# Performance work log

Measured on AMD Instinct MI355X. Metric: run time of the kernel, lower is better.

The kernel has to match this reference:

```python
import jax, jax.numpy as jnp
import numpy as np

L, H, NH, NKV, HD, FF, V = 2, 2048, 16, 2, 128, 11008, 32000
B, S, R, LORA_SCALE = 32, 64, 16, 2.0  # lora scaling = alpha/r = 32/16
PH, TD = 1024, 512
ROPE_THETA = 1e6

def _rms(x, w, eps=1e-6):
    return x * jax.lax.rsqrt(jnp.mean(x * x, axis=-1, keepdims=True) + eps) * w

def _rot_half(x):
    h = x.shape[-1] // 2
    return jnp.concatenate([-x[..., h:], x[..., :h]], axis=-1)

def _lora_linear(x, W, A, Bm, b=None):
    y = x @ W.T + LORA_SCALE * ((x @ A.T) @ Bm.T)
    return y + b if b is not None else y

def _forward(input_ids, attention_mask, embed, Wq, bq, Aq, Bq, Wk, bk, Ak, Bk,
             Wv, bv, Av, Bv, Wo, Ao, Bo, ln1, ln2, Wg, Wu, Wd, norm_f,
             W1, b1, W2, b2):
    Bsz, Sl = input_ids.shape
    h = embed[input_ids]                                            # [B,S,H]
    inv_freq = 1.0 / (ROPE_THETA ** (jnp.arange(0, HD, 2, dtype=jnp.float32) / HD))
    ang = jnp.arange(Sl, dtype=jnp.float32)[:, None] * inv_freq      # [S,HD/2]
    cos = jnp.concatenate([jnp.cos(ang)] * 2, -1)[None, :, None, :]  # [1,S,1,HD]
    sin = jnp.concatenate([jnp.sin(ang)] * 2, -1)[None, :, None, :]
    causal = jnp.tril(jnp.ones((Sl, Sl), dtype=bool))
    keep = causal[None, None] & (attention_mask[:, None, None, :] > 0)
    bias = jnp.where(keep, 0.0, -1e9).astype(jnp.float32)            # [B,1,S,S]
    for l in range(L):
        x = _rms(h, ln1[l])
        q = _lora_linear(x, Wq[l], Aq[l], Bq[l], bq[l]).reshape(Bsz, Sl, NH, HD)
        k = _lora_linear(x, Wk[l], Ak[l], Bk[l], bk[l]).reshape(Bsz, Sl, NKV, HD)
        v = _lora_linear(x, Wv[l], Av[l], Bv[l], bv[l]).reshape(Bsz, Sl, NKV, HD)
        q = q * cos + _rot_half(q) * sin
        k = k * cos + _rot_half(k) * sin
        k = jnp.repeat(k, NH // NKV, axis=2)                         # GQA expand
        v = jnp.repeat(v, NH // NKV, axis=2)
        scores = jnp.einsum('bqhd,bkhd->bhqk', q, k) / np.sqrt(HD).astype(np.float32) + bias
        p = jax.nn.softmax(scores, axis=-1)
        attn = jnp.einsum('bhqk,bkhd->bqhd', p, v).reshape(Bsz, Sl, H)
        h = h + _lora_linear(attn, Wo[l], Ao[l], Bo[l])
        x = _rms(h, ln2[l])
        h = h + (jax.nn.silu(x @ Wg[l].T) * (x @ Wu[l].T)) @ Wd[l].T  # SwiGLU MLP
    h = _rms(h, norm_f)                       # final norm -> hidden_states[-1]
    seq_len = jnp.sum(attention_mask, axis=1) - 1
    pooled = h[jnp.arange(Bsz), seq_len]      # last valid token  [B,H]
    z = jax.nn.gelu(pooled @ W1.T + b1, approximate=False)
    return (z @ W2.T + b2).astype(jnp.float32)  # [B,512]

def setup_inputs():
    key = jax.random.key(0)
    ks = jax.random.split(key, 32)
    def n(k, shape, s=0.02):
        return (s * jax.random.normal(k, shape)).astype(jnp.float32)
    lens = jax.random.randint(ks[0], (B,), 1, S + 1)
    return {
        'input_ids': jax.random.randint(ks[1], (B, S), 0, V, dtype=jnp.int32),
        'attention_mask': (jnp.arange(S)[None, :] < lens[:, None]).astype(jnp.int32),
        'embed': n(ks[2], (V, H)),
        'Wq': n(ks[3], (L, H, H)), 'bq': n(ks[4], (L, H)),
        'Aq': n(ks[5], (L, R, H)), 'Bq': n(ks[6], (L, H, R)),
        'Wk': n(ks[7], (L, NKV * HD, H)), 'bk': n(ks[8], (L, NKV * HD)),
        'Ak': n(ks[9], (L, R, H)), 'Bk': n(ks[10], (L, NKV * HD, R)),
        'Wv': n(ks[11], (L, NKV * HD, H)), 'bv': n(ks[12], (L, NKV * HD)),
        'Av': n(ks[13], (L, R, H)), 'Bv': n(ks[14], (L, NKV * HD, R)),
        'Wo': n(ks[15], (L, H, H)),
        'Ao': n(ks[16], (L, R, H)), 'Bo': n(ks[17], (L, H, R)),
        'ln1': jnp.ones((L, H), jnp.float32), 'ln2': jnp.ones((L, H), jnp.float32),
        'Wg': n(ks[18], (L, FF, H)), 'Wu': n(ks[19], (L, FF, H)), 'Wd': n(ks[20], (L, H, FF)),
        'norm_f': jnp.ones((H,), jnp.float32),
        'W1': n(ks[21], (PH, H)), 'b1': jnp.zeros((PH,), jnp.float32),
        'W2': n(ks[22], (TD, PH)), 'b2': jnp.zeros((TD,), jnp.float32),
    }

def reference(input_ids, attention_mask, embed, Wq, bq, Aq, Bq, Wk, bk, Ak, Bk,
              Wv, bv, Av, Bv, Wo, Ao, Bo, ln1, ln2, Wg, Wu, Wd, norm_f,
              W1, b1, W2, b2):
    return _forward(input_ids, attention_mask, embed, Wq, bq, Aq, Bq, Wk, bk, Ak, Bk,
                    Wv, bv, Av, Bv, Wo, Ao, Bo, ln1, ln2, Wg, Wu, Wd, norm_f,
                    W1, b1, W2, b2)
```

## Files before the change

### kernel.cpp

```cpp
#include <hip/hip_runtime.h>
#include <hip/hip_bf16.h>
#include <math.h>

namespace {
constexpr int NL  = 2;
constexpr int H   = 2048;
constexpr int NH  = 16;
constexpr int NKV = 2;
constexpr int HD  = 128;
constexpr int FF  = 11008;
constexpr int BB  = 32;
constexpr int SS  = 64;
constexpr int RR  = 16;
constexpr int TT  = BB * SS;
constexpr int KVD = NKV * HD;
constexpr int QKVD = H + 2 * KVD;
constexpr int PH  = 1024, TDm = 512;
constexpr float LSCALE = 2.0f;
}

typedef __bf16 bf16x8 __attribute__((ext_vector_type(8)));
typedef float  f32x4  __attribute__((ext_vector_type(4)));

__device__ __forceinline__ ushort4 f4_to_bf4(float4 r) {
  __hip_bfloat16 a = __float2bfloat16(r.x), b = __float2bfloat16(r.y),
                 c = __float2bfloat16(r.z), d = __float2bfloat16(r.w);
  return make_ushort4(*(unsigned short*)&a, *(unsigned short*)&b,
                      *(unsigned short*)&c, *(unsigned short*)&d);
}

__device__ __forceinline__ bf16x8 f8cvt(float4 a, float4 b) {
  bf16x8 r;
  r[0] = (__bf16)a.x; r[1] = (__bf16)a.y; r[2] = (__bf16)a.z; r[3] = (__bf16)a.w;
  r[4] = (__bf16)b.x; r[5] = (__bf16)b.y; r[6] = (__bf16)b.z; r[7] = (__bf16)b.w;
  return r;
}

__device__ __forceinline__ float dot4(float4 a, float4 b) {
  return a.x * b.x + a.y * b.y + a.z * b.z + a.w * b.w;
}

__global__ __launch_bounds__(256) void k_embed(const int* __restrict__ ids,
                                               const float* __restrict__ emb,
                                               float* __restrict__ h) {
  int t = blockIdx.x;
  long id = ids[t];
  const float4* src = reinterpret_cast<const float4*>(emb + id * (long)H);
  float4* dst = reinterpret_cast<float4*>(h + (long)t * H);
  for (int i = threadIdx.x; i < H / 4; i += 256) dst[i] = src[i];
}

__global__ __launch_bounds__(256) void k_cvt(const float* __restrict__ src,
                                             __hip_bfloat16* __restrict__ dst, long n) {
  long i = ((long)blockIdx.x * 256 + threadIdx.x) * 4;
  if (i >= n) return;
  float4 v = *reinterpret_cast<const float4*>(src + i);
  *reinterpret_cast<ushort4*>(dst + i) = f4_to_bf4(v);
}

__global__ __launch_bounds__(256) void k_prep(
    const float* __restrict__ bq, const float* __restrict__ bk, const float* __restrict__ bv,
    const float* __restrict__ Bq, const float* __restrict__ Bk, const float* __restrict__ Bv,
    float* __restrict__ biascat, float* __restrict__ bcat) {
  int idx = blockIdx.x * 256 + threadIdx.x;
  if (idx >= NL * QKVD) return;
  int l = idx / QKVD, col = idx % QKVD;
  const float* bsrc; const float* Bsrc;
  if (col < H)            { bsrc = bq + (long)l * H + col;            Bsrc = Bq + ((long)l * H + col) * RR; }
  else if (col < H + KVD) { bsrc = bk + (long)l * KVD + (col - H);    Bsrc = Bk + ((long)l * KVD + col - H) * RR; }
  else                    { bsrc = bv + (long)l * KVD + (col - H - KVD); Bsrc = Bv + ((long)l * KVD + col - H - KVD) * RR; }
  biascat[idx] = *bsrc;
  #pragma unroll
  for (int r = 0; r < RR; ++r) bcat[(long)idx * RR + r] = Bsrc[r];
}

__global__ __launch_bounds__(256) void k_rmsnorm(const float* __restrict__ in,
                                                 const float* __restrict__ w,
                                                 float* __restrict__ out,
                                                 __hip_bfloat16* __restrict__ outb) {
  int t = blockIdx.x, tid = threadIdx.x;
  const float4* xr = reinterpret_cast<const float4*>(in + (long)t * H);
  float4 v0 = xr[tid], v1 = xr[tid + 256];
  float ss = v0.x*v0.x + v0.y*v0.y + v0.z*v0.z + v0.w*v0.w
           + v1.x*v1.x + v1.y*v1.y + v1.z*v1.z + v1.w*v1.w;
  #pragma unroll
  for (int off = 32; off; off >>= 1) ss += __shfl_xor(ss, off);
  __shared__ float sred[4];
  if ((tid & 63) == 0) sred[tid >> 6] = ss;
  __syncthreads();
  float scale = rsqrtf((sred[0] + sred[1] + sred[2] + sred[3]) * (1.0f / H) + 1e-6f);
  const float4* wr = reinterpret_cast<const float4*>(w);
  float4 w0 = wr[tid], w1 = wr[tid + 256];
  float4 r0 = make_float4(v0.x*scale*w0.x, v0.y*scale*w0.y, v0.z*scale*w0.z, v0.w*scale*w0.w);
  float4 r1 = make_float4(v1.x*scale*w1.x, v1.y*scale*w1.y, v1.z*scale*w1.z, v1.w*scale*w1.w);
  float4* o = reinterpret_cast<float4*>(out + (long)t * H);
  o[tid] = r0; o[tid + 256] = r1;
  ushort4* ob = reinterpret_cast<ushort4*>(outb + (long)t * H);
  ob[tid] = f4_to_bf4(r0); ob[tid + 256] = f4_to_bf4(r1);
}

enum { ME_BIAS_F32 = 0, ME_ACC_F32 = 1 };

__device__ __forceinline__ int raster_sw(int bid, int nwg) {
  int q8 = nwg >> 3, r8 = nwg & 7;
  int xcd = bid & 7, pos = bid >> 3;
  return (xcd < r8 ? xcd * (q8 + 1) : r8 * (q8 + 1) + (xcd - r8) * q8) + pos;
}

template <int EPI, bool LORA, bool WBF16>
__global__ __launch_bounds__(256, 3) void k_mgemm(
    const __hip_bfloat16* __restrict__ Abf,
    const float* __restrict__ W0, const float* __restrict__ W1, const float* __restrict__ W2,
    const __hip_bfloat16* __restrict__ Wb,
    const float* __restrict__ bias,
    float* __restrict__ Cf,
    const float* __restrict__ lt, const float* __restrict__ lB, int ltStride,
    int qkvMode, int M, int N, int K) {
  constexpr int BM = 64, BN = 128, BK = 64;
  constexpr int FM = 4, FN = 2;
  __shared__ __align__(16) __bf16 As[2][BM * BK];
  __shared__ __align__(16) __bf16 Bs[2][BN * BK];
  const int tid = threadIdx.x;
  const int sw = raster_sw(blockIdx.x, gridDim.x);
  const int ntm = M / BM;
  const int bm = (sw % ntm) * BM, bn = (sw / ntm) * BN;
  const int lane = tid & 63, wv = tid >> 6;
  const int wn = wv * 32;
  const int lr15 = lane & 15;
  const int g4 = lane >> 4;
  f32x4 acc[FM][FN] = {};
  const __bf16* Ag = reinterpret_cast<const __bf16*>(Abf) + (long)bm * K;

  const float* Wsrc = W0; int wrow0 = bn;
  if constexpr (!WBF16) {
    if (qkvMode) {
      if (bn >= H + KVD)      { Wsrc = W2; wrow0 = bn - (H + KVD); }
      else if (bn >= H)       { Wsrc = W1; wrow0 = bn - H; }
    }
  }
  const __bf16* Wg16 = reinterpret_cast<const __bf16*>(Wb) + (long)bn * K;

  const int arow = tid >> 3, acol = tid & 7;

  auto stageA = [&](int buf, int k0) {
    __builtin_amdgcn_global_load_lds(
        (const __attribute__((address_space(1))) void*)
          (Ag + (long)arow * K + k0 + ((acol ^ (arow & 7)) << 3)),
        (__attribute__((address_space(3))) void*)(&As[buf][tid * 8]), 16, 0, 0);
    int r1 = arow + 32;
    __builtin_amdgcn_global_load_lds(
        (const __attribute__((address_space(1))) void*)
          (Ag + (long)r1 * K + k0 + ((acol ^ (r1 & 7)) << 3)),
        (__attribute__((address_space(3))) void*)(&As[buf][(tid + 256) * 8]), 16, 0, 0);
  };

  auto stageB16 = [&](int buf, int k0) {
    #pragma unroll
    for (int q = 0; q < 4; ++q) {
      int c = tid + q * 256;
      int row = c >> 3, col = c & 7;
      __builtin_amdgcn_global_load_lds(
          (const __attribute__((address_space(1))) void*)
            (Wg16 + (long)row * K + k0 + ((col ^ (row & 7)) << 3)),
          (__attribute__((address_space(3))) void*)(&Bs[buf][c * 8]), 16, 0, 0);
    }
  };

  float4 bb[4][2];
  auto loadB = [&](int k0) {
    #pragma unroll
    for (int q = 0; q < 4; ++q) {
      int r = arow + q * 32;
      const float* p = Wsrc + (long)(wrow0 + r) * K + k0 + ((acol ^ (r & 7)) << 3);
      bb[q][0] = *reinterpret_cast<const float4*>(p);
      bb[q][1] = *reinterpret_cast<const float4*>(p + 4);
    }
  };
  auto writeB = [&](int buf) {
    #pragma unroll
    for (int q = 0; q < 4; ++q)
      *reinterpret_cast<bf16x8*>(&Bs[buf][(tid + q * 256) * 8]) = f8cvt(bb[q][0], bb[q][1]);
  };

  auto compute = [&](int buf) {
    #pragma unroll
    for (int ks = 0; ks < 2; ++ks) {
      bf16x8 af[FM], bfr[FN];
      #pragma unroll
      for (int m = 0; m < FM; ++m) {
        int row = m * 16 + lr15;
        af[m] = *reinterpret_cast<const bf16x8*>(
            &As[buf][row * BK + (((g4 + 4 * ks) ^ (row & 7)) << 3)]);
      }
      #pragma unroll
      for (int n = 0; n < FN; ++n) {
        int row = wn + n * 16 + lr15;
        bfr[n] = *reinterpret_cast<const bf16x8*>(
            &Bs[buf][row * BK + (((g4 + 4 * ks) ^ (row & 7)) << 3)]);
      }
      #pragma unroll
      for (int m = 0; m < FM; ++m)
        #pragma unroll
        for (int n = 0; n < FN; ++n)
          acc[m][n] = __builtin_amdgcn_mfma_f32_16x16x32_bf16(af[m], bfr[n], acc[m][n], 0, 0, 0);
    }
  };

  const int NS = K / BK;
  if constexpr (WBF16) {
    stageA(0, 0); stageB16(0, 0);
    __syncthreads();
    int cur = 0;
    for (int t = 0; t < NS; ++t) {
      if (t + 1 < NS) { stageA(cur ^ 1, (t + 1) * BK); stageB16(cur ^ 1, (t + 1) * BK); }
      compute(cur);
      if (t + 1 < NS) { __syncthreads(); cur ^= 1; }
    }
  } else {
    loadB(0);
    stageA(0, 0);
    writeB(0);
    __syncthreads();
    int cur = 0;
    for (int t = 0; t < NS; ++t) {
      if (t + 1 < NS) { loadB((t + 1) * BK); stageA(cur ^ 1, (t + 1) * BK); }
      compute(cur);
      if (t + 1 < NS) {
        writeB(cur ^ 1);
        __syncthreads();
        cur ^= 1;
      }
    }
  }

  const int r0 = g4 << 2;
  float4 lb[FN][4];
  int goff = 0;
  if constexpr (LORA) {
    if (qkvMode) goff = (bn >= H + KVD) ? 32 : (bn >= H ? 16 : 0);
    #pragma unroll
    for (int n = 0; n < FN; ++n) {
      const float4* p = reinterpret_cast<const float4*>(lB + (long)(bn + wn + n * 16 + lr15) * RR);
      lb[n][0] = p[0]; lb[n][1] = p[1]; lb[n][2] = p[2]; lb[n][3] = p[3];
    }
  }
  float bcol[FN];
  if constexpr (EPI == ME_BIAS_F32) {
    #pragma unroll
    for (int n = 0; n < FN; ++n) bcol[n] = bias[bn + wn + n * 16 + lr15];
  }
  #pragma unroll
  for (int m = 0; m < FM; ++m)
    #pragma unroll
    for (int j = 0; j < 4; ++j) {
      const long row = bm + m * 16 + r0 + j;
      float lv[FN];
      if constexpr (LORA) {
        const float4* tp = reinterpret_cast<const float4*>(lt + row * ltStride + goff);
        float4 t0 = tp[0], t1 = tp[1], t2 = tp[2], t3 = tp[3];
        #pragma unroll
        for (int n = 0; n < FN; ++n)
          lv[n] = LSCALE * (dot4(t0, lb[n][0]) + dot4(t1, lb[n][1]) +
                            dot4(t2, lb[n][2]) + dot4(t3, lb[n][3]));
      }
      #pragma unroll
      for (int n = 0; n < FN; ++n) {
        const int col = bn + wn + n * 16 + lr15;
        float v = acc[m][n][j];
        if constexpr (LORA) v += lv[n];
        if constexpr (EPI == ME_BIAS_F32) Cf[row * N + col] = v + bcol[n];
        else                              Cf[row * N + col] += v;
      }
    }
}

__global__ __launch_bounds__(256, 2) void k_swiglu_b(
    const __hip_bfloat16* __restrict__ Abf,
    const __hip_bfloat16* __restrict__ Wgb,
    const __hip_bfloat16* __restrict__ Wub,
    __hip_bfloat16* __restrict__ Cb,
    int M, int N, int K) {
  constexpr int BM = 128, BN = 128, BK = 32;
  constexpr int FM = 4, FN = 4;
  constexpr int ACH = BM * BK / 8;
  __shared__ __align__(16) __bf16 As[2][BM * BK];
  __shared__ __align__(16) __bf16 Gs[2][BN * BK];
  __shared__ __align__(16) __bf16 Us[2][BN * BK];
  const int tid = threadIdx.x;
  const int sw = raster_sw(blockIdx.x, gridDim.x);
  const int ntm = M / BM;
  const int bm = (sw % ntm) * BM, bn = (sw / ntm) * BN;
  const int lane = tid & 63, wv = tid >> 6;
  const int wm = (wv >> 1) * 64, wn = (wv & 1) * 64;
  const int lr15 = lane & 15;
  const int lks = (((lane >> 4) << 3)) ^ ((((lr15 >> 1) & 3)) << 3);
  f32x4 accg[FM][FN] = {}, accu[FM][FN] = {};
  const __bf16* Ag = reinterpret_cast<const __bf16*>(Abf) + (long)bm * K;
  const __bf16* Gg = reinterpret_cast<const __bf16*>(Wgb) + (long)bn * K;
  const __bf16* Ug = reinterpret_cast<const __bf16*>(Wub) + (long)bn * K;

  auto stage = [&](int buf, int k0) {
    #pragma unroll
    for (int i = tid; i < ACH; i += 256) {
      const int sc = ((i & 3) ^ ((i >> 3) & 3)) << 3;
      const long ro = (long)(i >> 2) * K + k0 + sc;
      __builtin_amdgcn_global_load_lds(
          (const __attribute__((address_space(1))) void*)(Ag + ro),
          (__attribute__((address_space(3))) void*)(&As[buf][i * 8]), 16, 0, 0);
      __builtin_amdgcn_global_load_lds(
          (const __attribute__((address_space(1))) void*)(Gg + ro),
          (__attribute__((address_space(3))) void*)(&Gs[buf][i * 8]), 16, 0, 0);
      __builtin_amdgcn_global_load_lds(
          (const __attribute__((address_space(1))) void*)(Ug + ro),
          (__attribute__((address_space(3))) void*)(&Us[buf][i * 8]), 16, 0, 0);
    }
  };
  auto compute = [&](int buf) {
    bf16x8 af[FM], gf[FN], uf[FN];
    #pragma unroll
    for (int m = 0; m < FM; ++m)
      af[m] = *reinterpret_cast<const bf16x8*>(&As[buf][(wm + m * 16 + lr15) * BK + lks]);
    #pragma unroll
    for (int n = 0; n < FN; ++n) {
      gf[n] = *reinterpret_cast<const bf16x8*>(&Gs[buf][(wn + n * 16 + lr15) * BK + lks]);
      uf[n] = *reinterpret_cast<const bf16x8*>(&Us[buf][(wn + n * 16 + lr15) * BK + lks]);
    }
    #pragma unroll
    for (int m = 0; m < FM; ++m)
      #pragma unroll
      for (int n = 0; n < FN; ++n) {
        accg[m][n] = __builtin_amdgcn_mfma_f32_16x16x32_bf16(af[m], gf[n], accg[m][n], 0, 0, 0);
        accu[m][n] = __builtin_amdgcn_mfma_f32_16x16x32_bf16(af[m], uf[n], accu[m][n], 0, 0, 0);
      }
  };

  const int NS = K / BK;
  stage(0, 0);
  asm volatile("s_waitcnt vmcnt(0)" ::: "memory");
  __builtin_amdgcn_s_barrier();
  int cur = 0;
  for (int t = 0; t < NS; ++t) {
    if (t + 1 < NS) stage(cur ^ 1, (t + 1) * BK);
    compute(cur);
    if (t + 1 < NS) {
      asm volatile("s_waitcnt vmcnt(0)" ::: "memory");
      __builtin_amdgcn_s_barrier();
      cur ^= 1;
    }
  }

  const int r0 = (lane >> 4) << 2;
  #pragma unroll
  for (int m = 0; m < FM; ++m)
    #pragma unroll
    for (int n = 0; n < FN; ++n) {
      const int col = bn + wn + n * 16 + lr15;
      const long rowb = bm + wm + m * 16 + r0;
      #pragma unroll
      for (int j = 0; j < 4; ++j) {
        float g = accg[m][n][j], u = accu[m][n][j];
        Cb[(rowb + j) * N + col] = __float2bfloat16((g / (1.0f + expf(-g))) * u);
      }
    }
}

__global__ __launch_bounds__(256, 2) void k_swiglu(
    const __hip_bfloat16* __restrict__ Abf,
    const float* __restrict__ Wg,
    const float* __restrict__ Wu,
    __hip_bfloat16* __restrict__ Cb,
    int M, int N, int K) {
  constexpr int BM = 128, BN = 128, BK = 32;
  constexpr int FM = 4, FN = 4;
  __shared__ __align__(16) __bf16 As[2][BM * BK];
  __shared__ __align__(16) __bf16 Gs[2][BN * BK];
  __shared__ __align__(16) __bf16 Us[2][BN * BK];
  const int tid = threadIdx.x;
  const int sw = raster_sw(blockIdx.x, gridDim.x);
  const int ntm = M / BM;
  const int bm = (sw % ntm) * BM, bn = (sw / ntm) * BN;
  const int lane = tid & 63, wv = tid >> 6;
  const int wm = (wv >> 1) * 64, wn = (wv & 1) * 64;
  const int lr15 = lane & 15;
  const int lks = (((lane >> 4) << 3)) ^ ((((lr15 >> 1) & 3)) << 3);
  f32x4 accg[FM][FN] = {}, accu[FM][FN] = {};
  const __bf16* Ag = reinterpret_cast<const __bf16*>(Abf) + (long)bm * K;

  const int br0 = tid >> 2, bc = tid & 3;
  const int br1 = br0 + 64;
  const float* gp0 = Wg + (long)(bn + br0) * K + bc * 8;
  const float* gp1 = Wg + (long)(bn + br1) * K + bc * 8;
  const float* up0 = Wu + (long)(bn + br0) * K + bc * 8;
  const float* up1 = Wu + (long)(bn + br1) * K + bc * 8;
  const int d0 = br0 * BK + ((bc ^ ((br0 >> 1) & 3)) << 3);
  const int d1 = br1 * BK + ((bc ^ ((br1 >> 1) & 3)) << 3);

  float4 g00, g01, g10, g11, u00, u01, u10, u11;
  auto loadB = [&](int k0) {
    g00 = *reinterpret_cast<const float4*>(gp0 + k0);
    g01 = *reinterpret_cast<const float4*>(gp0 + k0 + 4);
    g10 = *reinterpret_cast<const float4*>(gp1 + k0);
    g11 = *reinterpret_cast<const float4*>(gp1 + k0 + 4);
    u00 = *reinterpret_cast<const float4*>(up0 + k0);
    u01 = *reinterpret_cast<const float4*>(up0 + k0 + 4);
    u10 = *reinterpret_cast<const float4*>(up1 + k0);
    u11 = *reinterpret_cast<const float4*>(up1 + k0 + 4);
  };
  auto writeB = [&](int buf) {
    *reinterpret_cast<bf16x8*>(&Gs[buf][d0]) = f8cvt(g00, g01);
    *reinterpret_cast<bf16x8*>(&Gs[buf][d1]) = f8cvt(g10, g11);
    *reinterpret_cast<bf16x8*>(&Us[buf][d0]) = f8cvt(u00, u01);
    *reinterpret_cast<bf16x8*>(&Us[buf][d1]) = f8cvt(u10, u11);
  };
  auto stageA = [&](int buf, int k0) {
    #pragma unroll
    for (int i = tid; i < BM * BK / 8; i += 256)
      __builtin_amdgcn_global_load_lds(
          (const __attribute__((address_space(1))) void*)
            (Ag + (long)(i >> 2) * K + k0 + (((i & 3) ^ ((i >> 3) & 3)) << 3)),
          (__attribute__((address_space(3))) void*)(&As[buf][i * 8]), 16, 0, 0);
  };
  auto compute = [&](int buf) {
    bf16x8 af[FM], gf[FN], uf[FN];
    #pragma unroll
    for (int m = 0; m < FM; ++m)
      af[m] = *reinterpret_cast<const bf16x8*>(&As[buf][(wm + m * 16 + lr15) * BK + lks]);
    #pragma unroll
    for (int n = 0; n < FN; ++n) {
      gf[n] = *reinterpret_cast<const bf16x8*>(&Gs[buf][(wn + n * 16 + lr15) * BK + lks]);
      uf[n] = *reinterpret_cast<const bf16x8*>(&Us[buf][(wn + n * 16 + lr15) * BK + lks]);
    }
    #pragma unroll
    for (int m = 0; m < FM; ++m)
      #pragma unroll
      for (int n = 0; n < FN; ++n) {
        accg[m][n] = __builtin_amdgcn_mfma_f32_16x16x32_bf16(af[m], gf[n], accg[m][n], 0, 0, 0);
        accu[m][n] = __builtin_amdgcn_mfma_f32_16x16x32_bf16(af[m], uf[n], accu[m][n], 0, 0, 0);
      }
  };

  const int NS = K / BK;
  loadB(0);
  stageA(0, 0);
  writeB(0);
  __syncthreads();
  int cur = 0;
  for (int t = 0; t < NS; ++t) {
    if (t + 1 < NS) { loadB((t + 1) * BK); stageA(cur ^ 1, (t + 1) * BK); }
    compute(cur);
    if (t + 1 < NS) {
      writeB(cur ^ 1);
      __syncthreads();
      cur ^= 1;
    }
  }

  const int r0 = (lane >> 4) << 2;
  #pragma unroll
  for (int m = 0; m < FM; ++m)
    #pragma unroll
    for (int n = 0; n < FN; ++n) {
      const int col = bn + wn + n * 16 + lr15;
      const long rowb = bm + wm + m * 16 + r0;
      #pragma unroll
      for (int j = 0; j < 4; ++j) {
        float g = accg[m][n][j], u = accu[m][n][j];
        Cb[(rowb + j) * N + col] = __float2bfloat16((g / (1.0f + expf(-g))) * u);
      }
    }
}

enum { EPI_STORE = 0, EPI_GELU = 3 };

template <int EPI, bool HAS_BIAS>
__global__ __launch_bounds__(256) void k_gemm(const float* __restrict__ A,
                                              const float* __restrict__ W,
                                              const float* __restrict__ bias,
                                              float* __restrict__ C,
                                              int M, int N, int K) {
  constexpr int BM = 64, BN = 64, BK = 16;
  __shared__ float As[BK][BM + 4];
  __shared__ float Ws[BK][BN + 4];
  const int bm = blockIdx.y * BM, bn = blockIdx.x * BN;
  const int tid = threadIdx.x;
  const int lr = tid >> 2;
  const int lc = (tid & 3) << 2;
  const int ty = tid >> 4, tx = tid & 15;
  float acc[4][4] = {};
  const int arow = bm + lr;
  const bool aok = arow < M;
  const float* Ap = A + (long)arow * K + lc;
  const float* Wp = W + (long)(bn + lr) * K + lc;
  for (int k0 = 0; k0 < K; k0 += BK) {
    float4 av = aok ? *reinterpret_cast<const float4*>(Ap + k0) : make_float4(0.f, 0.f, 0.f, 0.f);
    float4 wv = *reinterpret_cast<const float4*>(Wp + k0);
    As[lc + 0][lr] = av.x; As[lc + 1][lr] = av.y; As[lc + 2][lr] = av.z; As[lc + 3][lr] = av.w;
    Ws[lc + 0][lr] = wv.x; Ws[lc + 1][lr] = wv.y; Ws[lc + 2][lr] = wv.z; Ws[lc + 3][lr] = wv.w;
    __syncthreads();
    #pragma unroll
    for (int k = 0; k < BK; ++k) {
      float4 a4 = *reinterpret_cast<const float4*>(&As[k][ty << 2]);
      float4 b4 = *reinterpret_cast<const float4*>(&Ws[k][tx << 2]);
      float a[4] = {a4.x, a4.y, a4.z, a4.w};
      float b[4] = {b4.x, b4.y, b4.z, b4.w};
      #pragma unroll
      for (int i = 0; i < 4; ++i)
        #pragma unroll
        for (int j = 0; j < 4; ++j) acc[i][j] = fmaf(a[i], b[j], acc[i][j]);
    }
    __syncthreads();
  }
  const int col = bn + (tx << 2);
  #pragma unroll
  for (int i = 0; i < 4; ++i) {
    int row = bm + (ty << 2) + i;
    if (row < M) {
      float4 r = make_float4(acc[i][0], acc[i][1], acc[i][2], acc[i][3]);
      if (HAS_BIAS) {
        float4 bv = *reinterpret_cast<const float4*>(bias + col);
        r.x += bv.x; r.y += bv.y; r.z += bv.z; r.w += bv.w;
      }
      if (EPI == EPI_GELU) {
        r.x = 0.5f * r.x * (1.0f + erff(r.x * 0.70710678118654752f));
        r.y = 0.5f * r.y * (1.0f + erff(r.y * 0.70710678118654752f));
        r.z = 0.5f * r.z * (1.0f + erff(r.z * 0.70710678118654752f));
        r.w = 0.5f * r.w * (1.0f + erff(r.w * 0.70710678118654752f));
      }
      *reinterpret_cast<float4*>(C + (long)row * N + col) = r;
    }
  }
}

__global__ __launch_bounds__(256) void k_lora_down3(
    const float* __restrict__ x,
    const float* __restrict__ A0, const float* __restrict__ A1, const float* __restrict__ A2,
    float* __restrict__ out, int outStride) {
  int t = blockIdx.x, g = blockIdx.y, tid = threadIdx.x;
  const float* A = (g == 0) ? A0 : (g == 1) ? A1 : A2;
  int r = tid & 15, sl = tid >> 4;
  const float* xr = x + (long)t * H + sl * 128;
  const float* Ar = A + (long)r * H + sl * 128;
  float p = 0.f;
  #pragma unroll 8
  for (int kk = 0; kk < 128; kk += 4) {
    float4 xv = *reinterpret_cast<const float4*>(xr + kk);
    float4 av = *reinterpret_cast<const float4*>(Ar + kk);
    p = fmaf(xv.x, av.x, p); p = fmaf(xv.y, av.y, p);
    p = fmaf(xv.z, av.z, p); p = fmaf(xv.w, av.w, p);
  }
  __shared__ float red[16][17];
  red[sl][r] = p;
  __syncthreads();
  if (tid < 16) {
    float s = 0.f;
    #pragma unroll
    for (int i = 0; i < 16; ++i) s += red[i][tid];
    out[(long)t * outStride + g * 16 + tid] = s;
  }
}

__global__ __launch_bounds__(256) void k_rope_tab(float2* __restrict__ tab) {
  int idx = blockIdx.x * 256 + threadIdx.x;
  if (idx >= SS * 64) return;
  int pos = idx >> 6, j = idx & 63;
  float inv = 1.0f / powf(1.0e6f, (float)(2 * j) * (1.0f / HD));
  float ang = (float)pos * inv;
  tab[idx] = make_float2(cosf(ang), sinf(ang));
}

__global__ __launch_bounds__(256) void k_rope(float* __restrict__ qkv,
                                              const float2* __restrict__ tab) {
  int t = blockIdx.x;
  const float2* trow = tab + (t & (SS - 1)) * 64;
  float* row = qkv + (long)t * QKVD;
  for (int idx = threadIdx.x; idx < NH * 64 + NKV * 64; idx += 256) {
    float* base;
    int j;
    if (idx < NH * 64) {
      int head = idx >> 6; j = idx & 63;
      base = row + head * HD;
    } else {
      int i2 = idx - NH * 64;
      int head = i2 >> 6; j = i2 & 63;
      base = row + H + head * HD;
    }
    float2 cs2 = trow[j];
    float lo = base[j], hi = base[j + 64];
    base[j]      = lo * cs2.x - hi * cs2.y;
    base[j + 64] = hi * cs2.x + lo * cs2.y;
  }
}

__global__ __launch_bounds__(64) void k_attn(const float* __restrict__ qkv,
                                             const int* __restrict__ mask,
                                             float* __restrict__ o,
                                             __hip_bfloat16* __restrict__ obf) {
  int flat = blockIdx.x;
  int qi = flat & (SS - 1);
  int hh = (flat >> 6) & (NH - 1);
  int b  = flat >> 10;
  int lane = threadIdx.x;
  int kv = hh >> 3;
  long t = (long)b * SS + qi;
  const float* qr = qkv + t * QKVD + hh * HD;
  const float* kr = qkv + ((long)b * SS + lane) * QKVD + H + kv * HD;
  float dot = 0.f;
  #pragma unroll 8
  for (int d = 0; d < HD; d += 4) {
    float4 qv = *reinterpret_cast<const float4*>(qr + d);
    float4 kvv = *reinterpret_cast<const float4*>(kr + d);
    dot = fmaf(qv.x, kvv.x, dot); dot = fmaf(qv.y, kvv.y, dot);
    dot = fmaf(qv.z, kvv.z, dot); dot = fmaf(qv.w, kvv.w, dot);
  }
  bool keep = (lane <= qi) && (mask[b * SS + lane] > 0);
  float sc = dot * 0.08838834764831845f + (keep ? 0.f : -1e9f);
  float m = sc;
  #pragma unroll
  for (int off = 32; off; off >>= 1) m = fmaxf(m, __shfl_xor(m, off));
  float e = expf(sc - m);
  float s = e;
  #pragma unroll
  for (int off = 32; off; off >>= 1) s += __shfl_xor(s, off);
  float p = e / s;
  __shared__ float pl[64];
  pl[lane] = p;
  __syncthreads();
  float o0 = 0.f, o1 = 0.f;
  const float* vb = qkv + (long)b * SS * QKVD + H + KVD + kv * HD;
  for (int ki = 0; ki < SS; ++ki) {
    float pp = pl[ki];
    o0 = fmaf(pp, vb[(long)ki * QKVD + lane], o0);
    o1 = fmaf(pp, vb[(long)ki * QKVD + lane + 64], o1);
  }
  long oidx = t * H + hh * HD + lane;
  o[oidx] = o0;
  o[oidx + 64] = o1;
  __hip_bfloat16 b0 = __float2bfloat16(o0), b1 = __float2bfloat16(o1);
  obf[oidx] = b0;
  obf[oidx + 64] = b1;
}

__global__ __launch_bounds__(256) void k_pool(const float* __restrict__ x,
                                              const int* __restrict__ mask,
                                              float* __restrict__ pooled) {
  int b = blockIdx.x;
  __shared__ int len;
  if (threadIdx.x == 0) {
    int L2 = 0;
    for (int i = 0; i < SS; ++i) L2 += (mask[b * SS + i] > 0);
    len = L2;
  }
  __syncthreads();
  const float4* sp = reinterpret_cast<const float4*>(x + ((long)b * SS + len - 1) * H);
  float4* dp = reinterpret_cast<float4*>(pooled + (long)b * H);
  for (int i = threadIdx.x; i < H / 4; i += 256) dp[i] = sp[i];
}

static inline int cvt_grid(long n) { return (int)((n / 4 + 255) / 256); }

extern "C" void kernel_launch(void* const* d_in, const int* in_sizes, int n_in,
                              void* d_out, int out_size, void* d_ws, size_t ws_size,
                              hipStream_t stream) {
  const int*   ids    = (const int*)d_in[0];
  const int*   mask   = (const int*)d_in[1];
  const float* embed  = (const float*)d_in[2];
  const float* Wq     = (const float*)d_in[3];
  const float* bq     = (const float*)d_in[4];
  const float* Aq     = (const float*)d_in[5];
  const float* Bq     = (const float*)d_in[6];
  const float* Wk     = (const float*)d_in[7];
  const float* bk     = (const float*)d_in[8];
  const float* Ak     = (const float*)d_in[9];
  const float* Bk     = (const float*)d_in[10];
  const float* Wv     = (const float*)d_in[11];
  const float* bv     = (const float*)d_in[12];
  const float* Av     = (const float*)d_in[13];
  const float* Bv     = (const float*)d_in[14];
  const float* Wo     = (const float*)d_in[15];
  const float* Ao     = (const float*)d_in[16];
  const float* Bo     = (const float*)d_in[17];
  const float* ln1    = (const float*)d_in[18];
  const float* ln2    = (const float*)d_in[19];
  const float* Wg     = (const float*)d_in[20];
  const float* Wu     = (const float*)d_in[21];
  const float* Wd     = (const float*)d_in[22];
  const float* norm_f = (const float*)d_in[23];
  const float* W1     = (const float*)d_in[24];
  const float* b1     = (const float*)d_in[25];
  const float* W2     = (const float*)d_in[26];
  const float* b2     = (const float*)d_in[27];

  float* ws = (float*)d_ws;
  float* h        = ws;
  float* x        = h    + (long)TT * H;
  float* qkv      = x    + (long)TT * H;
  float* tmpR     = qkv  + (long)TT * QKVD;
  float* tmpO     = tmpR + (long)TT * 48;
  float* pooled   = tmpO + (long)TT * 16;
  float* zz       = pooled + (long)BB * H;
  float* biascat  = zz   + (long)BB * PH;
  float* bcat     = biascat + (long)NL * QKVD;
  float2* ropetab = (float2*)(bcat + (long)NL * QKVD * RR);
  float* endf32   = (float*)(ropetab + SS * 64);
  __hip_bfloat16* x_bf  = (__hip_bfloat16*)endf32;
  __hip_bfloat16* ffbf  = x_bf + (long)TT * H;
  __hip_bfloat16* wgbf  = ffbf + (long)TT * FF;
  __hip_bfloat16* wubf  = wgbf + (long)FF * H;
  __hip_bfloat16* wdbf  = wubf + (long)FF * H;
  __hip_bfloat16* wqbf  = wdbf + (long)FF * H;
  __hip_bfloat16* wobf  = wqbf + (long)QKVD * H;
  size_t need_bf = (size_t)((char*)(wobf + (long)H * H) - (char*)d_ws);
  bool bfw = ws_size >= need_bf;

  k_embed<<<TT, 256, 0, stream>>>(ids, embed, h);
  k_rope_tab<<<(SS * 64 + 255) / 256, 256, 0, stream>>>(ropetab);
  k_prep<<<(NL * QKVD + 255) / 256, 256, 0, stream>>>(bq, bk, bv, Bq, Bk, Bv, biascat, bcat);

  for (int l = 0; l < NL; ++l) {
    const long lHH = (long)l * H * H;
    const long lKH = (long)l * KVD * H;
    const long lRH = (long)l * RR * H;
    const long lFH = (long)l * FF * H;
    k_rmsnorm<<<TT, 256, 0, stream>>>(h, ln1 + l * H, x, x_bf);
    k_lora_down3<<<dim3(TT, 3), 256, 0, stream>>>(
        x, Aq + lRH, Ak + lRH, Av + lRH, tmpR, 48);
    if (bfw) {
      k_cvt<<<cvt_grid((long)H * H), 256, 0, stream>>>(Wq + lHH, wqbf, (long)H * H);
      k_cvt<<<cvt_grid((long)KVD * H), 256, 0, stream>>>(Wk + lKH, wqbf + (long)H * H, (long)KVD * H);
      k_cvt<<<cvt_grid((long)KVD * H), 256, 0, stream>>>(Wv + lKH, wqbf + (long)(H + KVD) * H, (long)KVD * H);
      k_mgemm<ME_BIAS_F32, true, true><<<(TT / 64) * (QKVD / 128), 256, 0, stream>>>(
          x_bf, nullptr, nullptr, nullptr, wqbf, biascat + (long)l * QKVD, qkv,
          tmpR, bcat + (long)l * QKVD * RR, 48, 1, TT, QKVD, H);
    } else {
      k_mgemm<ME_BIAS_F32, true, false><<<(TT / 64) * (QKVD / 128), 256, 0, stream>>>(
          x_bf, Wq + lHH, Wk + lKH, Wv + lKH, nullptr, biascat + (long)l * QKVD, qkv,
          tmpR, bcat + (long)l * QKVD * RR, 48, 1, TT, QKVD, H);
    }
    k_rope<<<TT, 256, 0, stream>>>(qkv, ropetab);
    k_attn<<<BB * NH * SS, 64, 0, stream>>>(qkv, mask, x, x_bf);
    k_lora_down3<<<dim3(TT, 1), 256, 0, stream>>>(
        x, Ao + lRH, Ao + lRH, Ao + lRH, tmpO, 16);
    if (bfw) {
      k_cvt<<<cvt_grid((long)H * H), 256, 0, stream>>>(Wo + lHH, wobf, (long)H * H);
      k_mgemm<ME_ACC_F32, true, true><<<(TT / 64) * (H / 128), 256, 0, stream>>>(
          x_bf, nullptr, nullptr, nullptr, wobf, nullptr, h,
          tmpO, Bo + (long)l * H * RR, 16, 0, TT, H, H);
    } else {
      k_mgemm<ME_ACC_F32, true, false><<<(TT / 64) * (H / 128), 256, 0, stream>>>(
          x_bf, Wo + lHH, Wo + lHH, Wo + lHH, nullptr, nullptr, h,
          tmpO, Bo + (long)l * H * RR, 16, 0, TT, H, H);
    }
    k_rmsnorm<<<TT, 256, 0, stream>>>(h, ln2 + l * H, x, x_bf);
    if (bfw) {
      k_cvt<<<cvt_grid((long)FF * H), 256, 0, stream>>>(Wg + lFH, wgbf, (long)FF * H);
      k_cvt<<<cvt_grid((long)FF * H), 256, 0, stream>>>(Wu + lFH, wubf, (long)FF * H);
      k_swiglu_b<<<(TT / 128) * (FF / 128), 256, 0, stream>>>(
          x_bf, wgbf, wubf, ffbf, TT, FF, H);
      k_cvt<<<cvt_grid((long)H * FF), 256, 0, stream>>>(Wd + lFH, wdbf, (long)H * FF);
      k_mgemm<ME_ACC_F32, false, true><<<(TT / 64) * (H / 128), 256, 0, stream>>>(
          ffbf, nullptr, nullptr, nullptr, wdbf, nullptr, h,
          nullptr, nullptr, 0, 0, TT, H, FF);
    } else {
      k_swiglu<<<(TT / 128) * (FF / 128), 256, 0, stream>>>(
          x_bf, Wg + lFH, Wu + lFH, ffbf, TT, FF, H);
      k_mgemm<ME_ACC_F32, false, false><<<(TT / 64) * (H / 128), 256, 0, stream>>>(
          ffbf, Wd + lFH, Wd + lFH, Wd + lFH, nullptr, nullptr, h,
          nullptr, nullptr, 0, 0, TT, H, FF);
    }
  }

  k_rmsnorm<<<TT, 256, 0, stream>>>(h, norm_f, x, x_bf);
  k_pool<<<BB, 256, 0, stream>>>(x, mask, pooled);
  k_gemm<EPI_GELU, true><<<dim3(PH / 64, 1), 256, 0, stream>>>(pooled, W1, b1, zz, BB, PH, H);
  k_gemm<EPI_STORE, true><<<dim3(TDm / 64, 1), 256, 0, stream>>>(zz, W2, b2, (float*)d_out, BB, TDm, PH);
}
```

Before: 2.002 ms.

## Fuse RoPE into tiled attention, merge weight casts, use wave-per-output head GEMM

```diff
diff --git a/kernel.cpp b/kernel.cpp
--- a/kernel.cpp
+++ b/kernel.cpp
@@ -55,6 +55,34 @@
   long i = ((long)blockIdx.x * 256 + threadIdx.x) * 4;
   if (i >= n) return;
   float4 v = *reinterpret_cast<const float4*>(src + i);
+  *reinterpret_cast<ushort4*>(dst + i) = f4_to_bf4(v);
+}
+
+__global__ __launch_bounds__(256) void k_cvt_qkv(
+    const float* __restrict__ Wq, const float* __restrict__ Wk,
+    const float* __restrict__ Wv, __hip_bfloat16* __restrict__ dst) {
+  long i = ((long)blockIdx.x * 256 + threadIdx.x) * 4;
+  const long n1 = (long)H * H, n2 = n1 + (long)KVD * H, nt = (long)QKVD * H;
+  if (i >= nt) return;
+  const float* src; long off;
+  if (i < n1)      { src = Wq; off = i; }
+  else if (i < n2) { src = Wk; off = i - n1; }
+  else             { src = Wv; off = i - n2; }
+  float4 v = *reinterpret_cast<const float4*>(src + off);
+  *reinterpret_cast<ushort4*>(dst + i) = f4_to_bf4(v);
+}
+
+__global__ __launch_bounds__(256) void k_cvt3(
+    const float* __restrict__ s0, const float* __restrict__ s1,
+    const float* __restrict__ s2, __hip_bfloat16* __restrict__ dst) {
+  long i = ((long)blockIdx.x * 256 + threadIdx.x) * 4;
+  const long n = (long)FF * H;
+  if (i >= 3 * n) return;
+  const float* src; long off;
+  if (i < n)          { src = s0; off = i; }
+  else if (i < 2 * n) { src = s1; off = i - n; }
+  else                { src = s2; off = i - 2 * n; }
+  float4 v = *reinterpret_cast<const float4*>(src + off);
   *reinterpret_cast<ushort4*>(dst + i) = f4_to_bf4(v);
 }
 
@@ -470,64 +498,31 @@
     }
 }
 
-enum { EPI_STORE = 0, EPI_GELU = 3 };
-
-template <int EPI, bool HAS_BIAS>
-__global__ __launch_bounds__(256) void k_gemm(const float* __restrict__ A,
-                                              const float* __restrict__ W,
-                                              const float* __restrict__ bias,
-                                              float* __restrict__ C,
-                                              int M, int N, int K) {
-  constexpr int BM = 64, BN = 64, BK = 16;
-  __shared__ float As[BK][BM + 4];
-  __shared__ float Ws[BK][BN + 4];
-  const int bm = blockIdx.y * BM, bn = blockIdx.x * BN;
-  const int tid = threadIdx.x;
-  const int lr = tid >> 2;
-  const int lc = (tid & 3) << 2;
-  const int ty = tid >> 4, tx = tid & 15;
-  float acc[4][4] = {};
-  const int arow = bm + lr;
-  const bool aok = arow < M;
-  const float* Ap = A + (long)arow * K + lc;
-  const float* Wp = W + (long)(bn + lr) * K + lc;
-  for (int k0 = 0; k0 < K; k0 += BK) {
-    float4 av = aok ? *reinterpret_cast<const float4*>(Ap + k0) : make_float4(0.f, 0.f, 0.f, 0.f);
-    float4 wv = *reinterpret_cast<const float4*>(Wp + k0);
-    As[lc + 0][lr] = av.x; As[lc + 1][lr] = av.y; As[lc + 2][lr] = av.z; As[lc + 3][lr] = av.w;
-    Ws[lc + 0][lr] = wv.x; Ws[lc + 1][lr] = wv.y; Ws[lc + 2][lr] = wv.z; Ws[lc + 3][lr] = wv.w;
-    __syncthreads();
-    #pragma unroll
-    for (int k = 0; k < BK; ++k) {
-      float4 a4 = *reinterpret_cast<const float4*>(&As[k][ty << 2]);
-      float4 b4 = *reinterpret_cast<const float4*>(&Ws[k][tx << 2]);
-      float a[4] = {a4.x, a4.y, a4.z, a4.w};
-      float b[4] = {b4.x, b4.y, b4.z, b4.w};
-      #pragma unroll
-      for (int i = 0; i < 4; ++i)
-        #pragma unroll
-        for (int j = 0; j < 4; ++j) acc[i][j] = fmaf(a[i], b[j], acc[i][j]);
-    }
-    __syncthreads();
-  }
-  const int col = bn + (tx << 2);
+template <bool GELU>
+__global__ __launch_bounds__(256) void k_hgemm(const float* __restrict__ A,
+                                               const float* __restrict__ W,
+                                               const float* __restrict__ bias,
+                                               float* __restrict__ C,
+                                               int M, int N, int K) {
+  int idx = blockIdx.x * 4 + (threadIdx.x >> 6);
+  if (idx >= M * N) return;
+  int b = idx / N, n = idx % N;
+  int lane = threadIdx.x & 63;
+  const float* a = A + (long)b * K;
+  const float* w = W + (long)n * K;
+  float s = 0.f;
+  for (int k = lane * 4; k < K; k += 256) {
+    float4 av = *reinterpret_cast<const float4*>(a + k);
+    float4 wv = *reinterpret_cast<const float4*>(w + k);
+    s = fmaf(av.x, wv.x, s); s = fmaf(av.y, wv.y, s);
+    s = fmaf(av.z, wv.z, s); s = fmaf(av.w, wv.w, s);
+  }
   #pragma unroll
-  for (int i = 0; i < 4; ++i) {
-    int row = bm + (ty << 2) + i;
-    if (row < M) {
-      float4 r = make_float4(acc[i][0], acc[i][1], acc[i][2], acc[i][3]);
-      if (HAS_BIAS) {
-        float4 bv = *reinterpret_cast<const float4*>(bias + col);
-        r.x += bv.x; r.y += bv.y; r.z += bv.z; r.w += bv.w;
-      }
-      if (EPI == EPI_GELU) {
-        r.x = 0.5f * r.x * (1.0f + erff(r.x * 0.70710678118654752f));
-        r.y = 0.5f * r.y * (1.0f + erff(r.y * 0.70710678118654752f));
-        r.z = 0.5f * r.z * (1.0f + erff(r.z * 0.70710678118654752f));
-        r.w = 0.5f * r.w * (1.0f + erff(r.w * 0.70710678118654752f));
-      }
-      *reinterpret_cast<float4*>(C + (long)row * N + col) = r;
-    }
+  for (int off = 32; off; off >>= 1) s += __shfl_xor(s, off);
+  if (lane == 0) {
+    float v = s + bias[n];
+    if (GELU) v = 0.5f * v * (1.0f + erff(v * 0.70710678118654752f));
+    C[idx] = v;
   }
 }
 
@@ -568,76 +563,72 @@
   tab[idx] = make_float2(cosf(ang), sinf(ang));
 }
 
-__global__ __launch_bounds__(256) void k_rope(float* __restrict__ qkv,
-                                              const float2* __restrict__ tab) {
-  int t = blockIdx.x;
-  const float2* trow = tab + (t & (SS - 1)) * 64;
-  float* row = qkv + (long)t * QKVD;
-  for (int idx = threadIdx.x; idx < NH * 64 + NKV * 64; idx += 256) {
-    float* base;
-    int j;
-    if (idx < NH * 64) {
-      int head = idx >> 6; j = idx & 63;
-      base = row + head * HD;
-    } else {
-      int i2 = idx - NH * 64;
-      int head = i2 >> 6; j = i2 & 63;
-      base = row + H + head * HD;
-    }
-    float2 cs2 = trow[j];
-    float lo = base[j], hi = base[j + 64];
-    base[j]      = lo * cs2.x - hi * cs2.y;
-    base[j + 64] = hi * cs2.x + lo * cs2.y;
-  }
-}
-
-__global__ __launch_bounds__(64) void k_attn(const float* __restrict__ qkv,
-                                             const int* __restrict__ mask,
-                                             float* __restrict__ o,
-                                             __hip_bfloat16* __restrict__ obf) {
-  int flat = blockIdx.x;
-  int qi = flat & (SS - 1);
-  int hh = (flat >> 6) & (NH - 1);
-  int b  = flat >> 10;
-  int lane = threadIdx.x;
-  int kv = hh >> 3;
-  long t = (long)b * SS + qi;
-  const float* qr = qkv + t * QKVD + hh * HD;
-  const float* kr = qkv + ((long)b * SS + lane) * QKVD + H + kv * HD;
-  float dot = 0.f;
-  #pragma unroll 8
-  for (int d = 0; d < HD; d += 4) {
-    float4 qv = *reinterpret_cast<const float4*>(qr + d);
-    float4 kvv = *reinterpret_cast<const float4*>(kr + d);
-    dot = fmaf(qv.x, kvv.x, dot); dot = fmaf(qv.y, kvv.y, dot);
-    dot = fmaf(qv.z, kvv.z, dot); dot = fmaf(qv.w, kvv.w, dot);
-  }
-  bool keep = (lane <= qi) && (mask[b * SS + lane] > 0);
-  float sc = dot * 0.08838834764831845f + (keep ? 0.f : -1e9f);
-  float m = sc;
-  #pragma unroll
-  for (int off = 32; off; off >>= 1) m = fmaxf(m, __shfl_xor(m, off));
-  float e = expf(sc - m);
-  float s = e;
-  #pragma unroll
-  for (int off = 32; off; off >>= 1) s += __shfl_xor(s, off);
-  float p = e / s;
-  __shared__ float pl[64];
-  pl[lane] = p;
+__global__ __launch_bounds__(256) void k_attn2(const float* __restrict__ qkv,
+                                               const int* __restrict__ mask,
+                                               const float2* __restrict__ tab,
+                                               float* __restrict__ o,
+                                               __hip_bfloat16* __restrict__ obf) {
+  __shared__ float Kt[128][65];
+  __shared__ float Vs[64][128];
+  __shared__ int   mb[64];
+  const int b = blockIdx.x, kv = blockIdx.y, qz = blockIdx.z;
+  const int tid = threadIdx.x, lane = tid & 63, wid = tid >> 6;
+  const float* kbase = qkv + ((long)b * SS) * QKVD + H + kv * HD;
+  for (int i = tid; i < 64 * 64; i += 256) {
+    int j = i & 63, ki = i >> 6;
+    const float* kr = kbase + (long)ki * QKVD;
+    float lo = kr[j], hi = kr[j + 64];
+    float2 cs = tab[ki * 64 + j];
+    Kt[j][ki]      = lo * cs.x - hi * cs.y;
+    Kt[j + 64][ki] = hi * cs.x + lo * cs.y;
+  }
+  const float* vbase = qkv + ((long)b * SS) * QKVD + H + KVD + kv * HD;
+  for (int i = tid; i < 64 * 32; i += 256) {
+    int f4 = i & 31, ki = i >> 5;
+    *reinterpret_cast<float4*>(&Vs[ki][f4 * 4]) =
+        *reinterpret_cast<const float4*>(vbase + (long)ki * QKVD + f4 * 4);
+  }
+  if (tid < 64) mb[tid] = mask[b * SS + tid];
   __syncthreads();
-  float o0 = 0.f, o1 = 0.f;
-  const float* vb = qkv + (long)b * SS * QKVD + H + KVD + kv * HD;
-  for (int ki = 0; ki < SS; ++ki) {
-    float pp = pl[ki];
-    o0 = fmaf(pp, vb[(long)ki * QKVD + lane], o0);
-    o1 = fmaf(pp, vb[(long)ki * QKVD + lane + 64], o1);
-  }
-  long oidx = t * H + hh * HD + lane;
-  o[oidx] = o0;
-  o[oidx + 64] = o1;
-  __hip_bfloat16 b0 = __float2bfloat16(o0), b1 = __float2bfloat16(o1);
-  obf[oidx] = b0;
-  obf[oidx + 64] = b1;
+
+  for (int rr = 0; rr < 32; ++rr) {
+    int br = wid * 32 + rr;
+    int qh = br >> 4, qi = qz * 16 + (br & 15);
+    int hh = kv * 8 + qh;
+    long t = (long)b * SS + qi;
+    const float* qr = qkv + t * QKVD + hh * HD;
+    float dot = 0.f;
+    #pragma unroll 8
+    for (int j = 0; j < 64; ++j) {
+      float2 cs = tab[qi * 64 + j];
+      float lo = qr[j], hi = qr[j + 64];
+      float rlo = lo * cs.x - hi * cs.y;
+      float rhi = hi * cs.x + lo * cs.y;
+      dot = fmaf(rlo, Kt[j][lane], dot);
+      dot = fmaf(rhi, Kt[j + 64][lane], dot);
+    }
+    bool keep = (lane <= qi) && (mb[lane] > 0);
+    float sc = dot * 0.08838834764831845f + (keep ? 0.f : -1e9f);
+    float m = sc;
+    #pragma unroll
+    for (int off = 32; off; off >>= 1) m = fmaxf(m, __shfl_xor(m, off));
+    float e = expf(sc - m);
+    float s = e;
+    #pragma unroll
+    for (int off = 32; off; off >>= 1) s += __shfl_xor(s, off);
+    float p = e / s;
+    float o0 = 0.f, o1 = 0.f;
+    #pragma unroll 8
+    for (int ki = 0; ki < 64; ++ki) {
+      float pk = __shfl(p, ki);
+      o0 = fmaf(pk, Vs[ki][lane], o0);
+      o1 = fmaf(pk, Vs[ki][lane + 64], o1);
+    }
+    long oidx = t * H + hh * HD + lane;
+    o[oidx] = o0; o[oidx + 64] = o1;
+    obf[oidx] = __float2bfloat16(o0);
+    obf[oidx + 64] = __float2bfloat16(o1);
+  }
 }
 
 __global__ __launch_bounds__(256) void k_pool(const float* __restrict__ x,
@@ -725,9 +716,8 @@
     k_lora_down3<<<dim3(TT, 3), 256, 0, stream>>>(
         x, Aq + lRH, Ak + lRH, Av + lRH, tmpR, 48);
     if (bfw) {
-      k_cvt<<<cvt_grid((long)H * H), 256, 0, stream>>>(Wq + lHH, wqbf, (long)H * H);
-      k_cvt<<<cvt_grid((long)KVD * H), 256, 0, stream>>>(Wk + lKH, wqbf + (long)H * H, (long)KVD * H);
-      k_cvt<<<cvt_grid((long)KVD * H), 256, 0, stream>>>(Wv + lKH, wqbf + (long)(H + KVD) * H, (long)KVD * H);
+      k_cvt_qkv<<<cvt_grid((long)QKVD * H), 256, 0, stream>>>(
+          Wq + lHH, Wk + lKH, Wv + lKH, wqbf);
       k_mgemm<ME_BIAS_F32, true, true><<<(TT / 64) * (QKVD / 128), 256, 0, stream>>>(
           x_bf, nullptr, nullptr, nullptr, wqbf, biascat + (long)l * QKVD, qkv,
           tmpR, bcat + (long)l * QKVD * RR, 48, 1, TT, QKVD, H);
@@ -736,8 +726,7 @@
           x_bf, Wq + lHH, Wk + lKH, Wv + lKH, nullptr, biascat + (long)l * QKVD, qkv,
           tmpR, bcat + (long)l * QKVD * RR, 48, 1, TT, QKVD, H);
     }
-    k_rope<<<TT, 256, 0, stream>>>(qkv, ropetab);
-    k_attn<<<BB * NH * SS, 64, 0, stream>>>(qkv, mask, x, x_bf);
+    k_attn2<<<dim3(BB, NKV, 4), 256, 0, stream>>>(qkv, mask, ropetab, x, x_bf);
     k_lora_down3<<<dim3(TT, 1), 256, 0, stream>>>(
         x, Ao + lRH, Ao + lRH, Ao + lRH, tmpO, 16);
     if (bfw) {
@@ -752,11 +741,10 @@
     }
     k_rmsnorm<<<TT, 256, 0, stream>>>(h, ln2 + l * H, x, x_bf);
     if (bfw) {
-      k_cvt<<<cvt_grid((long)FF * H), 256, 0, stream>>>(Wg + lFH, wgbf, (long)FF * H);
-      k_cvt<<<cvt_grid((long)FF * H), 256, 0, stream>>>(Wu + lFH, wubf, (long)FF * H);
+      k_cvt3<<<cvt_grid(3L * FF * H), 256, 0, stream>>>(
+          Wg + lFH, Wu + lFH, Wd + lFH, wgbf);
       k_swiglu_b<<<(TT / 128) * (FF / 128), 256, 0, stream>>>(
           x_bf, wgbf, wubf, ffbf, TT, FF, H);
-      k_cvt<<<cvt_grid((long)H * FF), 256, 0, stream>>>(Wd + lFH, wdbf, (long)H * FF);
       k_mgemm<ME_ACC_F32, false, true><<<(TT / 64) * (H / 128), 256, 0, stream>>>(
           ffbf, nullptr, nullptr, nullptr, wdbf, nullptr, h,
           nullptr, nullptr, 0, 0, TT, H, FF);
@@ -771,6 +759,6 @@
 
   k_rmsnorm<<<TT, 256, 0, stream>>>(h, norm_f, x, x_bf);
   k_pool<<<BB, 256, 0, stream>>>(x, mask, pooled);
-  k_gemm<EPI_GELU, true><<<dim3(PH / 64, 1), 256, 0, stream>>>(pooled, W1, b1, zz, BB, PH, H);
-  k_gemm<EPI_STORE, true><<<dim3(TDm / 64, 1), 256, 0, stream>>>(zz, W2, b2, (float*)d_out, BB, TDm, PH);
-}
+  k_hgemm<true><<<(BB * PH + 3) / 4, 256, 0, stream>>>(pooled, W1, b1, zz, BB, PH, H);
+  k_hgemm<false><<<(BB * TDm + 3) / 4, 256, 0, stream>>>(zz, W2, b2, (float*)d_out, BB, TDm, PH);
+}
```

Result: faster. 1.874 ms (median of 2 runs) (-6.4%).
